# Kernel tuning notes

Hardware: AMD Instinct MI355X
Metric: run time of the kernel (lower is better)

## Reference

```python
import jax, jax.numpy as jnp
import numpy as np

B, S, DIM, H, DH = 2, 2048, 1024, 16, 64
EPS = 1e-6


def rms_norm(x, w):
    # x: (..., DH); computed in fp32 like the torch module
    norm = jax.lax.rsqrt(jnp.mean(jnp.square(x), axis=-1, keepdims=True) + EPS)
    return (x * norm) * w


def apply_rope(x, freqs):
    # x: (B, H, S, D), freqs: (S, D); torch code slices cos/sin to first half
    d = x.shape[-1] // 2
    cos = jnp.cos(freqs)[None, None, :, :d]
    sin = jnp.sin(freqs)[None, None, :, :d]
    x1, x2 = x[..., :d], x[..., d:]
    return jnp.concatenate([x1 * cos - x2 * sin, x2 * cos + x1 * sin], axis=-1)


def setup_inputs() -> dict:
    key = jax.random.key(0)
    ks = jax.random.split(key, 4)
    x = jax.random.normal(ks[0], (B, S, DIM), dtype=jnp.float32)
    # causal additive mask
    causal = jnp.tril(jnp.ones((S, S), dtype=bool))
    mask = jnp.where(causal, 0.0, -1e9).astype(jnp.float32)[None, None]
    # standard rope frequencies: pos * inv_freq over head_dim
    inv_freq = 1.0 / (10000.0 ** (jnp.arange(0, DH, dtype=jnp.float32) / DH))
    rope_freqs = jnp.arange(S, dtype=jnp.float32)[:, None] * inv_freq[None, :]
    total = H * DH
    w_qkv = jax.random.normal(ks[1], (3 * total, DIM), dtype=jnp.float32) * (DIM ** -0.5)
    w_out = jax.random.normal(ks[2], (DIM, total), dtype=jnp.float32) * (total ** -0.5)
    q_norm_w = jnp.ones((DH,), dtype=jnp.float32)
    k_norm_w = jnp.ones((DH,), dtype=jnp.float32)
    return {"x": x, "mask": mask, "rope_freqs": rope_freqs, "w_qkv": w_qkv,
            "w_out": w_out, "q_norm_w": q_norm_w, "k_norm_w": k_norm_w}


def reference(x, mask, rope_freqs, w_qkv, w_out, q_norm_w, k_norm_w):
    b, s, _ = x.shape
    qkv = (x @ w_qkv.T).reshape(b, s, 3, H, DH)
    q, k, v = qkv[:, :, 0], qkv[:, :, 1], qkv[:, :, 2]
    q = jnp.transpose(rms_norm(q, q_norm_w), (0, 2, 1, 3))  # (B,H,S,DH)
    k = jnp.transpose(rms_norm(k, k_norm_w), (0, 2, 1, 3))
    v = jnp.transpose(v, (0, 2, 1, 3))
    q = apply_rope(q, rope_freqs)
    k = apply_rope(k, rope_freqs)
    scale = DH ** -0.5
    attn = jnp.einsum('bhsd,bhtd->bhst', q, k) * scale + mask
    attn = jax.nn.softmax(attn, axis=-1)
    out = jnp.einsum('bhst,bhtd->bhsd', attn, v)
    out = jnp.transpose(out, (0, 2, 1, 3)).reshape(b, s, H * DH)
    return out @ w_out.T
```

## Files before the change

### kernel.cpp

```cpp
#include <hip/hip_runtime.h>
#include <hip/hip_bf16.h>
#include <stdint.h>

typedef short bf16x8 __attribute__((ext_vector_type(8)));
typedef float f32x4  __attribute__((ext_vector_type(4)));

#define MFMA_BF16(a,b,c) __builtin_amdgcn_mfma_f32_16x16x32_bf16((a),(b),(c),0,0,0)

__device__ __forceinline__ void async_ld16(const void* g, void* l) {
  __builtin_amdgcn_global_load_lds(
      (const __attribute__((address_space(1))) void*)g,
      (__attribute__((address_space(3))) void*)l, 16, 0, 0);
}

__device__ __forceinline__ unsigned short bf16_bits(float x) {
  __hip_bfloat16 h = __float2bfloat16(x);
  return *(unsigned short*)&h;
}

#define NX_C    (2 * 2048 * 1024)
#define NWQKV_C (3072 * 1024)
#define NWOUT_C (1024 * 1024)

__global__ void __launch_bounds__(256)
cvt_all(const float* __restrict__ x, const float* __restrict__ wqkv,
        const float* __restrict__ wout, __hip_bfloat16* __restrict__ dst)
{
  const int i = (blockIdx.x * 256 + threadIdx.x) * 4;
  const float* src;
  int off;
  if (i < NX_C)                { src = x;    off = i; }
  else if (i < NX_C + NWQKV_C) { src = wqkv; off = i - NX_C; }
  else                         { src = wout; off = i - NX_C - NWQKV_C; }
  const float4 v = *(const float4*)(src + off);
  ushort4 u;
  u.x = bf16_bits(v.x); u.y = bf16_bits(v.y);
  u.z = bf16_bits(v.z); u.w = bf16_bits(v.w);
  *(ushort4*)((unsigned short*)dst + i) = u;
}

template<int EPI>
__global__ void __launch_bounds__(256)
gemm_bt(const __hip_bfloat16* __restrict__ A,
        const __hip_bfloat16* __restrict__ B,
        int K,
        __hip_bfloat16* __restrict__ o0,
        __hip_bfloat16* __restrict__ o1,
        __hip_bfloat16* __restrict__ o2,
        float* __restrict__ of,
        const float* __restrict__ freqs,
        const float* __restrict__ qw,
        const float* __restrict__ kw)
{
  __shared__ __align__(16) __hip_bfloat16 As[2][2][128 * 32];
  __shared__ __align__(16) __hip_bfloat16 Bs[2][2][64 * 32];

  const int tid  = threadIdx.x;
  const int w    = tid >> 6;
  const int lane = tid & 63;
  const int quad = lane >> 4;
  const int l15  = lane & 15;

  const int m0 = blockIdx.y * 128;
  const int n0 = blockIdx.x * 64;

  const int srow = lane >> 2;
  const int sgr  = ((lane & 3) ^ ((lane >> 3) & 3)) * 8;
  const int c0 = w * 2, c1 = w * 2 + 1;

  const int pg = l15 * 32 + (quad ^ ((l15 >> 1) & 3)) * 8;

  const int wm  = w * 32;
  const int ac0 = w * 2;

  f32x4 acc[2][4] = {};

#define GSTAGE(KN, BUF) do {                                                        \
    _Pragma("unroll")                                                               \
    for (int s_ = 0; s_ < 2; ++s_) {                                                \
      async_ld16(A + (size_t)(m0 + c0 * 16 + srow) * K + (KN) + 32 * s_ + sgr,      \
                 &As[BUF][s_][0] + c0 * 512);                                       \
      async_ld16(A + (size_t)(m0 + c1 * 16 + srow) * K + (KN) + 32 * s_ + sgr,      \
                 &As[BUF][s_][0] + c1 * 512);                                       \
      async_ld16(B + (size_t)(n0 + w * 16 + srow) * K + (KN) + 32 * s_ + sgr,       \
                 &Bs[BUF][s_][0] + w * 512);                                        \
    }                                                                               \
  } while (0)

  const int niter = K >> 6;
  GSTAGE(0, 0);

  for (int it = 0; it < niter; ++it) {
    const int cur = it & 1;
    __syncthreads();
    if (it + 1 < niter) GSTAGE((it + 1) << 6, cur ^ 1);

#pragma unroll
    for (int s = 0; s < 2; ++s) {
      const __hip_bfloat16* Ac = &As[cur][s][0];
      const __hip_bfloat16* Bc = &Bs[cur][s][0];
      bf16x8 af[2], bfr[4];
      af[0] = *(const bf16x8*)(Ac + (ac0 + 0) * 512 + pg);
      af[1] = *(const bf16x8*)(Ac + (ac0 + 1) * 512 + pg);
#pragma unroll
      for (int t = 0; t < 4; ++t)
        bfr[t] = *(const bf16x8*)(Bc + t * 512 + pg);
#pragma unroll
      for (int mt = 0; mt < 2; ++mt)
#pragma unroll
        for (int nt = 0; nt < 4; ++nt)
          acc[mt][nt] = MFMA_BF16(af[mt], bfr[nt], acc[mt][nt]);
    }
  }
#undef GSTAGE

  if (EPI == 1) {
    const int ldc = (int)gridDim.x * 64;
#pragma unroll
    for (int mt = 0; mt < 2; ++mt)
#pragma unroll
      for (int nt = 0; nt < 4; ++nt)
#pragma unroll
        for (int r = 0; r < 4; ++r)
          of[(size_t)(m0 + wm + mt * 16 + quad * 4 + r) * ldc
             + n0 + nt * 16 + l15] = acc[mt][nt][r];
    return;
  }

  const int which = n0 >> 10;
  const int hb    = (n0 & 1023) >> 6;

  if (which == 2) {
#pragma unroll
    for (int mt = 0; mt < 2; ++mt)
#pragma unroll
      for (int nt = 0; nt < 4; ++nt)
#pragma unroll
        for (int r = 0; r < 4; ++r) {
          const int m = m0 + wm + mt * 16 + quad * 4 + r;
          const int b = m >> 11, s = m & 2047;
          const int d = nt * 16 + l15;
          o2[((size_t)((b * 16 + hb) * 64 + d) << 11) + s] =
              __float2bfloat16(acc[mt][nt][r]);
        }
    return;
  }

  const float* wgt = which ? kw : qw;
  __hip_bfloat16* dst = which ? o1 : o0;
  const float wv0 = wgt[l15], wv1 = wgt[16 + l15];
  const float wv2 = wgt[32 + l15], wv3 = wgt[48 + l15];

#pragma unroll
  for (int mt = 0; mt < 2; ++mt) {
#pragma unroll
    for (int r = 0; r < 4; ++r) {
      float ssq = acc[mt][0][r] * acc[mt][0][r] + acc[mt][1][r] * acc[mt][1][r]
                + acc[mt][2][r] * acc[mt][2][r] + acc[mt][3][r] * acc[mt][3][r];
      ssq += __shfl_xor(ssq, 1);
      ssq += __shfl_xor(ssq, 2);
      ssq += __shfl_xor(ssq, 4);
      ssq += __shfl_xor(ssq, 8);
      float sc = rsqrtf(ssq * (1.0f / 64.0f) + 1e-6f);
      if (which == 0) sc *= 0.125f;

      const float y0 = acc[mt][0][r] * sc * wv0;
      const float y1 = acc[mt][1][r] * sc * wv1;
      const float y2 = acc[mt][2][r] * sc * wv2;
      const float y3 = acc[mt][3][r] * sc * wv3;

      const int m = m0 + wm + mt * 16 + quad * 4 + r;
      const int b = m >> 11, s = m & 2047;
      const float f0 = freqs[s * 64 + l15];
      const float f1 = freqs[s * 64 + 16 + l15];
      float sn0, cs0, sn1, cs1;
      __sincosf(f0, &sn0, &cs0);
      __sincosf(f1, &sn1, &cs1);

      const size_t row = ((size_t)((b * 16 + hb) * 2048 + s)) << 6;
      dst[row + l15]      = __float2bfloat16(y0 * cs0 - y2 * sn0);
      dst[row + 16 + l15] = __float2bfloat16(y1 * cs1 - y3 * sn1);
      dst[row + 32 + l15] = __float2bfloat16(y2 * cs0 + y0 * sn0);
      dst[row + 48 + l15] = __float2bfloat16(y3 * cs1 + y1 * sn1);
    }
  }
}

__global__ void __launch_bounds__(256, 2)
attn(const __hip_bfloat16* __restrict__ q,
     const __hip_bfloat16* __restrict__ k,
     const __hip_bfloat16* __restrict__ vt,
     __hip_bfloat16* __restrict__ ao)
{
  __shared__ __align__(16) __hip_bfloat16 Ks[2][2][64 * 64];
  __shared__ __align__(16) __hip_bfloat16 Vs[2][2][64 * 64];

  const int tid  = threadIdx.x;
  const int w    = tid >> 6;
  const int lane = tid & 63;
  const int quad = lane >> 4;
  const int l15  = lane & 15;

  const int lin  = blockIdx.x;
  const int c8   = lin & 7;
  const int rest = lin >> 3;
  const int pj   = rest & 15;
  const int bh   = ((rest >> 4) << 3) + c8;
  const int b    = bh >> 4, h = bh & 15;

  const __hip_bfloat16* qb = q  + (size_t)bh * 2048 * 64;
  const __hip_bfloat16* kb = k  + (size_t)bh * 2048 * 64;
  const __hip_bfloat16* vb = vt + (size_t)bh * 64 * 2048;

  const int pr = ((l15 >> 2) * 8) + (l15 & 3);

  const int pgk  = (quad ^ (l15 & 3) ^ (((l15 >> 2) & 1) << 2)) * 8;
  const int pgk4 = pgk ^ 32;
  const int pgv  = (quad ^ (l15 & 7)) * 8;
  const int pgv4 = pgv ^ 32;

  const int sj  = lane >> 3;
  const int sp  = lane & 7;
  const int kgA = (sp ^ (sj & 3)) * 8;
  const int kgB = kgA ^ 32;
  const int vgs = (sp ^ sj) * 8;
  const int ck0 = w * 2, ck1 = w * 2 + 1;

#define STAGE2(KEY0, BUF) do {                                                       \
    async_ld16(kb + (size_t)((KEY0) +      ck0 * 8 + sj) * 64 + kgA,                 \
               &Ks[BUF][0][0] + ck0 * 512);                                          \
    async_ld16(kb + (size_t)((KEY0) +      ck1 * 8 + sj) * 64 + kgB,                 \
               &Ks[BUF][0][0] + ck1 * 512);                                          \
    async_ld16(kb + (size_t)((KEY0) + 64 + ck0 * 8 + sj) * 64 + kgA,                 \
               &Ks[BUF][1][0] + ck0 * 512);                                          \
    async_ld16(kb + (size_t)((KEY0) + 64 + ck1 * 8 + sj) * 64 + kgB,                 \
               &Ks[BUF][1][0] + ck1 * 512);                                          \
    async_ld16(vb + (size_t)(ck0 * 8 + sj) * 2048 + (KEY0) +      vgs,               \
               &Vs[BUF][0][0] + ck0 * 512);                                          \
    async_ld16(vb + (size_t)(ck1 * 8 + sj) * 2048 + (KEY0) +      vgs,               \
               &Vs[BUF][0][0] + ck1 * 512);                                          \
    async_ld16(vb + (size_t)(ck0 * 8 + sj) * 2048 + (KEY0) + 64 + vgs,               \
               &Vs[BUF][1][0] + ck0 * 512);                                          \
    async_ld16(vb + (size_t)(ck1 * 8 + sj) * 2048 + (KEY0) + 64 + vgs,               \
               &Vs[BUF][1][0] + ck1 * 512);                                          \
  } while (0)

  for (int pass = 0; pass < 2; ++pass) {
    const int J  = pass ? (31 - pj) : pj;
    const int q0 = J * 64 + w * 16;
    const int qi = q0 + l15;

    const bf16x8 bq0 = *(const bf16x8*)(qb + (size_t)qi * 64 + quad * 8);
    const bf16x8 bq1 = *(const bf16x8*)(qb + (size_t)qi * 64 + 32 + quad * 8);

    f32x4 o[4] = {};
    float lsum = 0.f;

    const int ntile = (J >> 1) + 1;

    __syncthreads();
    STAGE2(0, 0);

    for (int kt = 0; kt < ntile; ++kt) {
      const int cur = kt & 1;

      __syncthreads();
      if (kt + 1 < ntile) STAGE2((kt + 1) * 128, cur ^ 1);

#pragma unroll
      for (int s = 0; s < 2; ++s) {
        const int su = kt * 2 + s;
        if (su > J) break;
        const int t0 = su * 64;
        const bool diag = (su == J);

        const __hip_bfloat16* Kc = &Ks[cur][s][0];
        const __hip_bfloat16* Vc = &Vs[cur][s][0];

        bf16x8 ka00, ka01, ka10, ka11, kb00, kb01, kb10, kb11;
        ka00 = *(const bf16x8*)(Kc + (pr)      * 64 + pgk);
        ka01 = *(const bf16x8*)(Kc + (pr)      * 64 + pgk4);
        ka10 = *(const bf16x8*)(Kc + (pr + 4)  * 64 + pgk);
        ka11 = *(const bf16x8*)(Kc + (pr + 4)  * 64 + pgk4);
        kb00 = *(const bf16x8*)(Kc + (32 + pr)     * 64 + pgk);
        kb01 = *(const bf16x8*)(Kc + (32 + pr)     * 64 + pgk4);
        kb10 = *(const bf16x8*)(Kc + (32 + pr + 4) * 64 + pgk);
        kb11 = *(const bf16x8*)(Kc + (32 + pr + 4) * 64 + pgk4);

        bf16x8 va[2][4];
#pragma unroll
        for (int dt = 0; dt < 4; ++dt) {
          va[0][dt] = *(const bf16x8*)(Vc + (dt * 16 + l15) * 64 + pgv);
          va[1][dt] = *(const bf16x8*)(Vc + (dt * 16 + l15) * 64 + pgv4);
        }

        f32x4 c00 = {}, c01 = {}, c10 = {}, c11 = {};
        c00 = MFMA_BF16(ka00, bq0, c00); c00 = MFMA_BF16(ka01, bq1, c00);
        c01 = MFMA_BF16(ka10, bq0, c01); c01 = MFMA_BF16(ka11, bq1, c01);
        c10 = MFMA_BF16(kb00, bq0, c10); c10 = MFMA_BF16(kb01, bq1, c10);
        c11 = MFMA_BF16(kb10, bq0, c11); c11 = MFMA_BF16(kb11, bq1, c11);

        float e00[4], e01[4], e10[4], e11[4];
#pragma unroll
        for (int r = 0; r < 4; ++r) {
          e00[r] = c00[r]; e01[r] = c01[r]; e10[r] = c10[r]; e11[r] = c11[r];
        }

        if (diag) {
#pragma unroll
          for (int r = 0; r < 4; ++r) {
            const int k0v = t0 + 8 * quad + r;
            if (k0v      > qi) e00[r] = -1e30f;
            if (k0v + 4  > qi) e01[r] = -1e30f;
            if (k0v + 32 > qi) e10[r] = -1e30f;
            if (k0v + 36 > qi) e11[r] = -1e30f;
          }
        }

        float rs = 0.f;
#pragma unroll
        for (int r = 0; r < 4; ++r) {
          e00[r] = __expf(e00[r] - 8.0f);
          e01[r] = __expf(e01[r] - 8.0f);
          e10[r] = __expf(e10[r] - 8.0f);
          e11[r] = __expf(e11[r] - 8.0f);
          rs += (e00[r] + e01[r]) + (e10[r] + e11[r]);
        }
        lsum += rs;

        bf16x8 pf0, pf1;
#pragma unroll
        for (int r = 0; r < 4; ++r) {
          pf0[r] = (short)bf16_bits(e00[r]);  pf0[r + 4] = (short)bf16_bits(e01[r]);
          pf1[r] = (short)bf16_bits(e10[r]);  pf1[r + 4] = (short)bf16_bits(e11[r]);
        }

#pragma unroll
        for (int dt = 0; dt < 4; ++dt) {
          o[dt] = MFMA_BF16(va[0][dt], pf0, o[dt]);
          o[dt] = MFMA_BF16(va[1][dt], pf1, o[dt]);
        }
      }
    }

    lsum += __shfl_xor(lsum, 16);
    lsum += __shfl_xor(lsum, 32);

    const float inv = 1.0f / lsum;
    const size_t row = ((size_t)(b * 2048 + qi)) * 1024 + h * 64;
#pragma unroll
    for (int dt = 0; dt < 4; ++dt) {
      ushort4 u;
      u.x = bf16_bits(o[dt][0] * inv);
      u.y = bf16_bits(o[dt][1] * inv);
      u.z = bf16_bits(o[dt][2] * inv);
      u.w = bf16_bits(o[dt][3] * inv);
      *(ushort4*)((unsigned short*)ao + row + dt * 16 + quad * 4) = u;
    }
  }
#undef STAGE2
}

extern "C" void kernel_launch(void* const* d_in, const int* in_sizes, int n_in,
                              void* d_out, int out_size, void* d_ws, size_t ws_size,
                              hipStream_t stream)
{
  const float* x    = (const float*)d_in[0];
  const float* rf   = (const float*)d_in[2];
  const float* wqkv = (const float*)d_in[3];
  const float* wout = (const float*)d_in[4];
  const float* qw   = (const float*)d_in[5];
  const float* kw   = (const float*)d_in[6];

  const size_t NE = (size_t)2 * 16 * 2048 * 64;

  __hip_bfloat16* qb  = (__hip_bfloat16*)d_ws;
  __hip_bfloat16* kb  = qb  + NE;
  __hip_bfloat16* vt  = kb  + NE;
  __hip_bfloat16* ao  = vt  + NE;
  __hip_bfloat16* xb  = ao  + NE;
  __hip_bfloat16* wqb = xb  + NX_C;
  __hip_bfloat16* wob = wqb + NWQKV_C;

  cvt_all<<<(NX_C + NWQKV_C + NWOUT_C) / 1024, 256, 0, stream>>>(x, wqkv, wout, xb);

  gemm_bt<0><<<dim3(48, 32), 256, 0, stream>>>(xb, wqb, 1024, qb, kb, vt,
                                               nullptr, rf, qw, kw);
  attn<<<512, 256, 0, stream>>>(qb, kb, vt, ao);
  gemm_bt<1><<<dim3(16, 32), 256, 0, stream>>>(ao, wob, 1024,
                                               nullptr, nullptr, nullptr, (float*)d_out,
                                               nullptr, nullptr, nullptr);
}
```

Measured before the change: 185.7 us.

## Use 512-thread attention blocks covering two adjacent query tiles per K/V stage

The attention kernel now launches 256 blocks of 8 waves instead of 512 blocks of 4 waves. Each block handles two consecutive 64-row query tiles, so every staged 128-key K/V chunk in shared memory is reused by twice as many waves. Each wave also issues half as many async loads, and global K/V traffic per query row drops. In exchange the lower-tile waves sit idle on the final key tile at the diagonal, there are fewer blocks to spread load across CUs, and the 512-thread launch bound with two blocks per CU may limit registers.

```diff
diff --git a/kernel.cpp b/kernel.cpp
--- a/kernel.cpp
+++ b/kernel.cpp
@@ -186,7 +186,7 @@
   }
 }
 
-__global__ void __launch_bounds__(256, 2)
+__global__ void __launch_bounds__(512, 2)
 attn(const __hip_bfloat16* __restrict__ q,
      const __hip_bfloat16* __restrict__ k,
      const __hip_bfloat16* __restrict__ vt,
@@ -204,8 +204,8 @@
   const int lin  = blockIdx.x;
   const int c8   = lin & 7;
   const int rest = lin >> 3;
-  const int pj   = rest & 15;
-  const int bh   = ((rest >> 4) << 3) + c8;
+  const int sp   = rest & 7;
+  const int bh   = ((rest >> 3) << 3) + c8;
   const int b    = bh >> 4, h = bh & 15;
 
   const __hip_bfloat16* qb = q  + (size_t)bh * 2048 * 64;
@@ -220,35 +220,26 @@
   const int pgv4 = pgv ^ 32;
 
   const int sj  = lane >> 3;
-  const int sp  = lane & 7;
-  const int kgA = (sp ^ (sj & 3)) * 8;
-  const int kgB = kgA ^ 32;
-  const int vgs = (sp ^ sj) * 8;
-  const int ck0 = w * 2, ck1 = w * 2 + 1;
+  const int spn = lane & 7;
+  const int kgA = (spn ^ (sj & 3)) * 8;
+  const int gK  = kgA ^ ((w & 1) << 5);
+  const int vgs = (spn ^ sj) * 8;
 
 #define STAGE2(KEY0, BUF) do {                                                       \
-    async_ld16(kb + (size_t)((KEY0) +      ck0 * 8 + sj) * 64 + kgA,                 \
-               &Ks[BUF][0][0] + ck0 * 512);                                          \
-    async_ld16(kb + (size_t)((KEY0) +      ck1 * 8 + sj) * 64 + kgB,                 \
-               &Ks[BUF][0][0] + ck1 * 512);                                          \
-    async_ld16(kb + (size_t)((KEY0) + 64 + ck0 * 8 + sj) * 64 + kgA,                 \
-               &Ks[BUF][1][0] + ck0 * 512);                                          \
-    async_ld16(kb + (size_t)((KEY0) + 64 + ck1 * 8 + sj) * 64 + kgB,                 \
-               &Ks[BUF][1][0] + ck1 * 512);                                          \
-    async_ld16(vb + (size_t)(ck0 * 8 + sj) * 2048 + (KEY0) +      vgs,               \
-               &Vs[BUF][0][0] + ck0 * 512);                                          \
-    async_ld16(vb + (size_t)(ck1 * 8 + sj) * 2048 + (KEY0) +      vgs,               \
-               &Vs[BUF][0][0] + ck1 * 512);                                          \
-    async_ld16(vb + (size_t)(ck0 * 8 + sj) * 2048 + (KEY0) + 64 + vgs,               \
-               &Vs[BUF][1][0] + ck0 * 512);                                          \
-    async_ld16(vb + (size_t)(ck1 * 8 + sj) * 2048 + (KEY0) + 64 + vgs,               \
-               &Vs[BUF][1][0] + ck1 * 512);                                          \
+    async_ld16(kb + (size_t)((KEY0) +      w * 8 + sj) * 64 + gK,                    \
+               &Ks[BUF][0][0] + w * 512);                                            \
+    async_ld16(kb + (size_t)((KEY0) + 64 + w * 8 + sj) * 64 + gK,                    \
+               &Ks[BUF][1][0] + w * 512);                                            \
+    async_ld16(vb + (size_t)(w * 8 + sj) * 2048 + (KEY0) +      vgs,                 \
+               &Vs[BUF][0][0] + w * 512);                                            \
+    async_ld16(vb + (size_t)(w * 8 + sj) * 2048 + (KEY0) + 64 + vgs,                 \
+               &Vs[BUF][1][0] + w * 512);                                            \
   } while (0)
 
   for (int pass = 0; pass < 2; ++pass) {
-    const int J  = pass ? (31 - pj) : pj;
-    const int q0 = J * 64 + w * 16;
-    const int qi = q0 + l15;
+    const int S  = pass ? (15 - sp) : sp;
+    const int Jw = 2 * S + (w >> 2);
+    const int qi = Jw * 64 + (w & 3) * 16 + l15;
 
     const bf16x8 bq0 = *(const bf16x8*)(qb + (size_t)qi * 64 + quad * 8);
     const bf16x8 bq1 = *(const bf16x8*)(qb + (size_t)qi * 64 + 32 + quad * 8);
@@ -256,7 +247,7 @@
     f32x4 o[4] = {};
     float lsum = 0.f;
 
-    const int ntile = (J >> 1) + 1;
+    const int ntile = S + 1;
 
     __syncthreads();
     STAGE2(0, 0);
@@ -270,9 +261,9 @@
 #pragma unroll
       for (int s = 0; s < 2; ++s) {
         const int su = kt * 2 + s;
-        if (su > J) break;
+        if (su > Jw) break;
         const int t0 = su * 64;
-        const bool diag = (su == J);
+        const bool diag = (su == Jw);
 
         const __hip_bfloat16* Kc = &Ks[cur][s][0];
         const __hip_bfloat16* Vc = &Vs[cur][s][0];
@@ -386,7 +377,7 @@
 
   gemm_bt<0><<<dim3(48, 32), 256, 0, stream>>>(xb, wqb, 1024, qb, kb, vt,
                                                nullptr, rf, qw, kw);
-  attn<<<512, 256, 0, stream>>>(qb, kb, vt, ao);
+  attn<<<256, 512, 0, stream>>>(qb, kb, vt, ao);
   gemm_bt<1><<<dim3(16, 32), 256, 0, stream>>>(ao, wob, 1024,
                                                nullptr, nullptr, nullptr, (float*)d_out,
                                                nullptr, nullptr, nullptr);
```

Result: no change. 186.3 us (+0.3%).
